# Optimization experiments

Measured on AMD Instinct MI355X. Metric: run time of the kernel, lower is better.

## Reference

```python
import jax, jax.numpy as jnp
import numpy as np

B_, H_, N_, L_ = 4, 512, 64, 2048  # batch, d_model, d_state/2 (conj pairs), seq len


def setup_inputs() -> dict:
    key = jax.random.key(0)
    ks = jax.random.split(key, 8)
    x = jax.random.normal(ks[0], (B_, H_, L_), jnp.float32)
    ln_w = jnp.ones((H_,), jnp.float32)
    ln_b = jnp.zeros((H_,), jnp.float32)
    # S4D-style init: dt log-uniform in [1e-3, 1e-1], A = -1/2 + i*pi*n (S4D-Lin)
    log_dt = jax.random.uniform(ks[1], (H_,), jnp.float32) * (np.log(0.1) - np.log(0.001)) + np.log(0.001)
    log_A_real = jnp.broadcast_to(jnp.log(jnp.float32(0.5)), (H_, N_))
    A_imag = jnp.broadcast_to(np.pi * jnp.arange(N_, dtype=np.float32), (H_, N_))
    B_re = jnp.ones((H_, N_), jnp.float32)
    B_im = jnp.zeros((H_, N_), jnp.float32)
    # 2 kernel channels for bidirectional
    C_re = jax.random.normal(ks[2], (2, H_, N_), jnp.float32) * (0.5 ** 0.5)
    C_im = jax.random.normal(ks[3], (2, H_, N_), jnp.float32) * (0.5 ** 0.5)
    D = jax.random.normal(ks[4], (H_,), jnp.float32)
    W_out = jax.random.normal(ks[5], (H_, H_), jnp.float32) / np.sqrt(H_)
    b_out = jnp.zeros((H_,), jnp.float32)
    return dict(x=x, ln_w=ln_w, ln_b=ln_b, log_dt=log_dt, log_A_real=log_A_real,
                A_imag=A_imag, B_re=B_re, B_im=B_im, C_re=C_re, C_im=C_im,
                D=D, W_out=W_out, b_out=b_out)


def _s4_layer(x, ln_w, ln_b, log_dt, log_A_real, A_imag, B_re, B_im, C_re, C_im, D, W_out, b_out):
    Bb, H, L = x.shape
    # ---- pre-norm LayerNorm over channel dim (module transposes to (B,L,H)) ----
    zt = x.transpose(0, 2, 1)                          # (B, L, H)
    mu = zt.mean(-1, keepdims=True)
    var = jnp.mean((zt - mu) ** 2, -1, keepdims=True)
    zt = (zt - mu) * jax.lax.rsqrt(var + 1e-5) * ln_w + ln_b
    z = zt.transpose(0, 2, 1)                          # (B, H, L)
    # ---- S4 diagonal SSM kernel, ZOH discretization, 2 channels (bidirectional) ----
    dt = jnp.exp(log_dt)[:, None]                      # (H, 1)
    A = -jnp.exp(log_A_real) + 1j * A_imag             # (H, N)
    dtA = A * dt                                       # (H, N)
    dB = (B_re + 1j * B_im) * (jnp.exp(dtA) - 1.0) / A # (H, N) discretized B
    CB = (C_re + 1j * C_im) * dB                       # (2, H, N)
    V = jnp.exp(dtA[:, :, None] * jnp.arange(L))       # (H, N, L) Vandermonde exp(l*dt*A)
    k = 2.0 * jnp.real(jnp.einsum('chn,hnl->chl', CB, V))  # (2, H, L)
    # ---- bidirectional: causal + flipped anticausal kernel, length 2L ----
    zpad = jnp.zeros_like(k[0])
    kb = jnp.concatenate([k[0], zpad], -1) + jnp.concatenate([zpad, k[1][:, ::-1]], -1)  # (H, 2L)
    # ---- FFT convolution ----
    k_f = jnp.fft.rfft(kb, n=2 * L)                    # (H, L+1)
    u_f = jnp.fft.rfft(z, n=2 * L)                     # (B, H, L+1)
    y = jnp.fft.irfft(u_f * k_f, n=2 * L)[..., :L]     # (B, H, L)
    y = y + z * D[:, None]                             # skip connection D*u
    y = jax.nn.gelu(y)                                 # default S4 activation
    y = jnp.einsum('oh,bhl->bol', W_out, y) + b_out[:, None]  # output linear (Conv1d k=1)
    return y + x                                       # residual of S4Layer


def reference(x, ln_w, ln_b, log_dt, log_A_real, A_imag, B_re, B_im, C_re, C_im, D, W_out, b_out):
    return _s4_layer(x, ln_w, ln_b, log_dt, log_A_real, A_imag, B_re, B_im, C_re, C_im, D, W_out, b_out)
```

## Files before the change

kernel.cpp:

```cpp
#include <hip/hip_runtime.h>
#include <math.h>

#define Bq 4
#define Hq 512
#define Nq 64
#define Lq 2048
#define PARAM (Hq*Nq)
#define T 64
#define NC (Lq/T)
#define NCOL 256

__global__ void prep_kernel(const float* __restrict__ log_dt,
                            const float* __restrict__ log_A_real,
                            const float* __restrict__ A_imag,
                            const float* __restrict__ B_re, const float* __restrict__ B_im,
                            const float* __restrict__ C_re, const float* __restrict__ C_im,
                            float* __restrict__ a0, float* __restrict__ b0,
                            float* __restrict__ a1, float* __restrict__ b1,
                            float* __restrict__ pw, float* __restrict__ pwT) {
    int idx = blockIdx.x * blockDim.x + threadIdx.x;
    if (idx >= PARAM) return;
    int h = idx >> 6, n = idx & 63;
    float dt = expf(log_dt[h]);
    float Ar = -expf(log_A_real[idx]);
    float Ai = A_imag[idx];
    float er = expf(Ar * dt);
    float wr = er * cosf(Ai * dt);
    float wi = er * sinf(Ai * dt);
    float mr = wr - 1.0f, mi = wi;
    float den = Ar * Ar + Ai * Ai;
    float qr = (mr * Ar + mi * Ai) / den;
    float qi = (mi * Ar - mr * Ai) / den;
    float Br = B_re[idx], Bi = B_im[idx];
    float dBr = Br * qr - Bi * qi;
    float dBi = Br * qi + Bi * qr;
    float cr = C_re[idx], ci = C_im[idx];
    a0[idx] =  2.0f * (cr * dBr - ci * dBi);
    b0[idx] = -2.0f * (cr * dBi + ci * dBr);
    cr = C_re[PARAM + idx]; ci = C_im[PARAM + idx];
    a1[idx] =  2.0f * (cr * dBr - ci * dBi);
    b1[idx] = -2.0f * (cr * dBi + ci * dBr);
    float c = 1.f, s = 0.f;
    float* base  = pw  + (size_t)h * 65 * 128 + 2 * n;
    float* baseT = pwT + (size_t)(h * 64 + n) * 132;
    for (int d = 0; d <= 64; ++d) {
        *(float2*)(base + (size_t)d * 128) = float2{c, s};
        *(float2*)(baseT + 2 * d)          = float2{c, s};
        float nc = c * wr - s * wi;
        float ns = c * wi + s * wr;
        c = nc; s = ns;
    }
}

__global__ __launch_bounds__(128)
void ktap_kernel(const float* __restrict__ pw,
                 const float* __restrict__ a0, const float* __restrict__ b0,
                 const float* __restrict__ a1, const float* __restrict__ b1,
                 float* __restrict__ kt) {
    int h = blockIdx.x;
    int t = threadIdx.x;
    int dir = t >> 6, d = t & 63;
    const float* aa = dir ? a1 : a0;
    const float* bb = dir ? b1 : b0;
    const float* row = pw + (size_t)(h * 65 + d) * 128;
    float acc = 0.f;
    for (int n = 0; n < 64; ++n) {
        float2 v = *(const float2*)(row + 2 * n);
        acc = fmaf(aa[h * 64 + n], v.x, acc);
        acc = fmaf(bb[h * 64 + n], v.y, acc);
    }
    kt[((size_t)h * 2 + dir) * 64 + d] = acc;
}

__global__ __launch_bounds__(256)
void ln_kernel(const float* __restrict__ x, const float* __restrict__ lnw,
               const float* __restrict__ lnb, float* __restrict__ z) {
    int blk = blockIdx.x;
    int b  = blk / (Lq / 16);
    int l0 = (blk % (Lq / 16)) * 16;
    int tx = threadIdx.x & 15;
    int ty = threadIdx.x >> 4;
    const float* xb = x + (size_t)b * Hq * Lq;
    float s = 0.f, s2 = 0.f;
    for (int h = ty; h < Hq; h += 16) {
        float v = xb[h * Lq + l0 + tx];
        s += v; s2 += v * v;
    }
    __shared__ float rs_[16][17], r2_[16][17], mu_s[16], sg_s[16];
    rs_[ty][tx] = s; r2_[ty][tx] = s2;
    __syncthreads();
    if (ty == 0) {
        float a = 0.f, c = 0.f;
        #pragma unroll
        for (int i = 0; i < 16; ++i) { a += rs_[i][tx]; c += r2_[i][tx]; }
        float mu = a * (1.0f / Hq);
        float var = c * (1.0f / Hq) - mu * mu;
        mu_s[tx] = mu;
        sg_s[tx] = rsqrtf(var + 1e-5f);
    }
    __syncthreads();
    float mu = mu_s[tx], rs = sg_s[tx];
    float* zb = z + (size_t)b * Hq * Lq;
    for (int h = ty; h < Hq; h += 16) {
        float v = xb[h * Lq + l0 + tx];
        zb[h * Lq + l0 + tx] = (v - mu) * rs * lnw[h] + lnb[h];
    }
}

__global__ __launch_bounds__(256, 6)
void delta_kernel(const float* __restrict__ z, const float* __restrict__ pw,
                  float* __restrict__ buf) {
    __shared__ float Bs[64][68];
    int h = blockIdx.x, ct = blockIdx.y;
    int t = threadIdx.x;
    int dir = ct >> 1;
    int cc = t & 31, rb = (t >> 5) & 1, jg = t >> 6;
    int b = (ct & 1) * 2 + rb;
    const float* zb = z + ((size_t)b * Hq + h) * Lq;
    if (dir == 0) {
        #pragma unroll
        for (int f = 0; f < 4; ++f) {
            float4 v = *(const float4*)(zb + cc * 64 + 16 * jg + 4 * f);
            Bs[16*jg+4*f+0][rb*32+cc] = v.x;
            Bs[16*jg+4*f+1][rb*32+cc] = v.y;
            Bs[16*jg+4*f+2][rb*32+cc] = v.z;
            Bs[16*jg+4*f+3][rb*32+cc] = v.w;
        }
    } else {
        #pragma unroll
        for (int f = 0; f < 4; ++f) {
            float4 v = *(const float4*)(zb + 2044 - cc * 64 - 16 * jg - 4 * f);
            Bs[16*jg+4*f+3][rb*32+cc] = v.x;
            Bs[16*jg+4*f+2][rb*32+cc] = v.y;
            Bs[16*jg+4*f+1][rb*32+cc] = v.z;
            Bs[16*jg+4*f+0][rb*32+cc] = v.w;
        }
    }
    __syncthreads();
    int tx = t & 15, ty = t >> 4;
    float aR[4][4] = {}, aI[4][4] = {};
    const float* pwh = pw + (size_t)h * 65 * 128;
    #pragma unroll 4
    for (int kk = 0; kk < 64; ++kk) {
        int d = 63 - kk;
        const float4* pr = (const float4*)(pwh + (size_t)d * 128 + 8 * tx);
        float4 p0 = pr[0], p1 = pr[1];
        float4 bv = *(const float4*)&Bs[kk][4 * ty];
        float pc[4] = {p0.x, p0.z, p1.x, p1.z};
        float ps[4] = {p0.y, p0.w, p1.y, p1.w};
        #pragma unroll
        for (int rr = 0; rr < 4; ++rr) {
            #pragma unroll
            for (int q = 0; q < 4; ++q) {
                aR[rr][q] = fmaf(pc[rr], (&bv.x)[q], aR[rr][q]);
                aI[rr][q] = fmaf(ps[rr], (&bv.x)[q], aI[rr][q]);
            }
        }
    }
    #pragma unroll
    for (int q = 0; q < 4; ++q) {
        int colg = ct * 64 + 4 * ty + q;
        float* dst = buf + ((size_t)h * NCOL + colg) * 128 + 8 * tx;
        float4 v1, v2;
        v1.x = aR[0][q]; v1.y = aI[0][q]; v1.z = aR[1][q]; v1.w = aI[1][q];
        v2.x = aR[2][q]; v2.y = aI[2][q]; v2.z = aR[3][q]; v2.w = aI[3][q];
        *(float4*)dst = v1; *(float4*)(dst + 4) = v2;
    }
}

__global__ __launch_bounds__(256)
void cscan_kernel(const float* __restrict__ pw, float* __restrict__ buf) {
    int e = blockIdx.x * 4 + (threadIdx.x >> 6);
    int n = threadIdx.x & 63;
    int h = e >> 3, dir = (e >> 2) & 1, b = e & 3;
    float2 t64 = *(const float2*)(pw + (size_t)(h * 65 + 64) * 128 + 2 * n);
    float tc = t64.x, ts = t64.y;
    float sr = 0.f, si = 0.f;
    float2* p = (float2*)(buf + ((size_t)h * NCOL + dir * 128 + b * 32) * 128) + n;
    float2 d = p[0];
    for (int c = 0; c < NC; ++c) {
        float2 dn;
        if (c + 1 < NC) dn = p[(c + 1) * 64];
        float2 s; s.x = sr; s.y = si;
        p[c * 64] = s;
        float nr = fmaf(tc, sr, fmaf(-ts, si, d.x));
        float ni = fmaf(ts, sr, fmaf(tc, si, d.y));
        sr = nr; si = ni; d = dn;
    }
}

__global__ __launch_bounds__(256, 4)
void yact_kernel(const float* __restrict__ z, const float* __restrict__ pwT,
                 const float* __restrict__ a0, const float* __restrict__ b0,
                 const float* __restrict__ a1, const float* __restrict__ b1,
                 const float* __restrict__ kt, const float* __restrict__ buf,
                 const float* __restrict__ Dv, float* __restrict__ u) {
    __shared__ float As[64][68];
    __shared__ float Bs[64][68];
    __shared__ float ks0[64], ks1[64], as0_[64], bs0_[64], as1_[64], bs1_[64];
    int h = blockIdx.x, bp = blockIdx.y;
    int t = threadIdx.x;
    if (t < 64) {
        ks0[t]  = kt[((size_t)h * 2 + 0) * 64 + t];
        ks1[t]  = kt[((size_t)h * 2 + 1) * 64 + t];
        as0_[t] = a0[h * 64 + t]; bs0_[t] = b0[h * 64 + t];
        as1_[t] = a1[h * 64 + t]; bs1_[t] = b1[h * 64 + t];
    }
    int tx = t & 15, ty = t >> 4;
    int si = t & 63, kg = t >> 6;
    int bS = 2 * bp + (si >> 5), ch = si & 31;
    const float* zb   = z + ((size_t)bS * Hq + h) * Lq + ch * 64;
    const float* bufh = buf + (size_t)h * NCOL * 128;
    const float* buf0 = bufh + (size_t)(bS * 32 + ch) * 128;
    const float* buf1 = bufh + (size_t)(128 + bS * 32 + (31 - ch)) * 128;
    const float* pwh  = pwT + (size_t)h * 64 * 132;
    float4 rB[4];
    float2 pv[8];
    #pragma unroll
    for (int f = 0; f < 4; ++f)
        rB[f] = *(const float4*)(zb + 16 * kg + 4 * f);
    float acc[4][4] = {};
    __syncthreads();
    for (int p = 0; p < 5; ++p) {
        if (p == 0) {
            #pragma unroll
            for (int q = 0; q < 16; ++q) {
                int kk = 16 * kg + q;
                int d = si - kk;
                As[kk][si] = (d >= 0) ? ks0[d] : ks1[-d - 1];
            }
        } else {
            const float* as_ = (p < 3) ? as0_ : as1_;
            const float* bs_ = (p < 3) ? bs0_ : bs1_;
            #pragma unroll
            for (int q = 0; q < 16; ++q) {
                int j = q >> 1;
                int n = 32 * ((p < 3) ? (p - 1) : (p - 3)) + 8 * kg + j;
                float vx = pv[j].x, vy = pv[j].y;
                As[16 * kg + q][si] = ((q & 1) == 0)
                    ? fmaf(as_[n], vx, bs_[n] * vy)
                    : fmaf(bs_[n], vx, -as_[n] * vy);
            }
        }
        #pragma unroll
        for (int f = 0; f < 4; ++f) {
            Bs[16*kg + 4*f + 0][si] = rB[f].x;
            Bs[16*kg + 4*f + 1][si] = rB[f].y;
            Bs[16*kg + 4*f + 2][si] = rB[f].z;
            Bs[16*kg + 4*f + 3][si] = rB[f].w;
        }
        __syncthreads();
        if (p < 4) {
            int pn = p + 1;
            int pp = (pn < 3) ? (pn - 1) : (pn - 3);
            const float* src = (pn < 3) ? buf0 : buf1;
            #pragma unroll
            for (int f = 0; f < 4; ++f)
                rB[f] = *(const float4*)(src + 64 * pp + 16 * kg + 4 * f);
            int dsel = (pn < 3) ? (si + 1) : (63 - si);
            #pragma unroll
            for (int j = 0; j < 8; ++j) {
                int n = 32 * pp + 8 * kg + j;
                pv[j] = *(const float2*)(pwh + (size_t)n * 132 + 2 * dsel);
            }
        }
        #pragma unroll 8
        for (int kk = 0; kk < 64; ++kk) {
            float4 av = *(const float4*)&As[kk][4 * tx];
            float4 bv = *(const float4*)&Bs[kk][4 * ty];
            #pragma unroll
            for (int ii = 0; ii < 4; ++ii) {
                float a = (&av.x)[ii];
                acc[ii][0] = fmaf(a, bv.x, acc[ii][0]);
                acc[ii][1] = fmaf(a, bv.y, acc[ii][1]);
                acc[ii][2] = fmaf(a, bv.z, acc[ii][2]);
                acc[ii][3] = fmaf(a, bv.w, acc[ii][3]);
            }
        }
        __syncthreads();
    }
    float dv = Dv[h];
    #pragma unroll
    for (int q = 0; q < 4; ++q) {
        int cc2 = 4 * ty + q;
        int b2 = 2 * bp + (cc2 >> 5), ch2 = cc2 & 31;
        size_t base = ((size_t)b2 * Hq + h) * Lq + ch2 * 64 + 4 * tx;
        float4 zr = *(const float4*)(z + base);
        float vv[4];
        vv[0] = acc[0][q] + dv * zr.x;
        vv[1] = acc[1][q] + dv * zr.y;
        vv[2] = acc[2][q] + dv * zr.z;
        vv[3] = acc[3][q] + dv * zr.w;
        #pragma unroll
        for (int i = 0; i < 4; ++i) {
            float v = vv[i];
            float tt = tanhf(0.7978845608028654f * (v + 0.044715f * v * v * v));
            vv[i] = 0.5f * v * (1.0f + tt);
        }
        float4 r; r.x = vv[0]; r.y = vv[1]; r.z = vv[2]; r.w = vv[3];
        *(float4*)(u + base) = r;
    }
}

__global__ __launch_bounds__(256, 1)
void gemm_kernel(const float* __restrict__ u, const float* __restrict__ W,
                 const float* __restrict__ bias, const float* __restrict__ x,
                 float* __restrict__ out) {
    __shared__ float Ws[2][32][132];
    __shared__ float Us[2][32][132];
    int l0 = blockIdx.x * 128;
    int o0 = blockIdx.y * 128;
    int b  = blockIdx.z;
    int t  = threadIdx.x;
    int tx = t & 15, ty = t >> 4;
    const float* ub = u + (size_t)b * Hq * Lq;
    int sf = t & 31, sk = t >> 5;
    int kq = t & 7,  ol = t >> 3;
    float4 su[4], sw[4];
    #pragma unroll
    for (int r = 0; r < 4; ++r)
        su[r] = *(const float4*)(ub + (size_t)(sk + 8*r) * Lq + l0 + 4*sf);
    #pragma unroll
    for (int r = 0; r < 4; ++r)
        sw[r] = *(const float4*)(W + (size_t)(o0 + ol + 32*r) * Hq + 4*kq);
    #pragma unroll
    for (int r = 0; r < 4; ++r)
        *(float4*)&Us[0][sk + 8*r][4*sf] = su[r];
    #pragma unroll
    for (int r = 0; r < 4; ++r) {
        Ws[0][4*kq+0][ol + 32*r] = sw[r].x;
        Ws[0][4*kq+1][ol + 32*r] = sw[r].y;
        Ws[0][4*kq+2][ol + 32*r] = sw[r].z;
        Ws[0][4*kq+3][ol + 32*r] = sw[r].w;
    }
    __syncthreads();
    float acc[2][4][2][4] = {};
    for (int kt = 0; kt < Hq / 32; ++kt) {
        int cur = kt & 1;
        if (kt < 15) {
            int k0 = (kt + 1) * 32;
            #pragma unroll
            for (int r = 0; r < 4; ++r)
                su[r] = *(const float4*)(ub + (size_t)(k0 + sk + 8*r) * Lq + l0 + 4*sf);
            #pragma unroll
            for (int r = 0; r < 4; ++r)
                sw[r] = *(const float4*)(W + (size_t)(o0 + ol + 32*r) * Hq + k0 + 4*kq);
        }
        #pragma unroll 4
        for (int k = 0; k < 32; ++k) {
            float4 a0v = *(const float4*)&Ws[cur][k][4 * tx];
            float4 a1v = *(const float4*)&Ws[cur][k][64 + 4 * tx];
            float4 b0v = *(const float4*)&Us[cur][k][4 * ty];
            float4 b1v = *(const float4*)&Us[cur][k][64 + 4 * ty];
            #pragma unroll
            for (int i = 0; i < 4; ++i) {
                float a0s = (&a0v.x)[i], a1s = (&a1v.x)[i];
                #pragma unroll
                for (int j = 0; j < 4; ++j) {
                    float b0s = (&b0v.x)[j], b1s = (&b1v.x)[j];
                    acc[0][i][0][j] = fmaf(a0s, b0s, acc[0][i][0][j]);
                    acc[0][i][1][j] = fmaf(a0s, b1s, acc[0][i][1][j]);
                    acc[1][i][0][j] = fmaf(a1s, b0s, acc[1][i][0][j]);
                    acc[1][i][1][j] = fmaf(a1s, b1s, acc[1][i][1][j]);
                }
            }
        }
        if (kt < 15) {
            int nxt = cur ^ 1;
            #pragma unroll
            for (int r = 0; r < 4; ++r)
                *(float4*)&Us[nxt][sk + 8*r][4*sf] = su[r];
            #pragma unroll
            for (int r = 0; r < 4; ++r) {
                Ws[nxt][4*kq+0][ol + 32*r] = sw[r].x;
                Ws[nxt][4*kq+1][ol + 32*r] = sw[r].y;
                Ws[nxt][4*kq+2][ol + 32*r] = sw[r].z;
                Ws[nxt][4*kq+3][ol + 32*r] = sw[r].w;
            }
        }
        __syncthreads();
    }
    #pragma unroll
    for (int oq = 0; oq < 2; ++oq) {
        #pragma unroll
        for (int i = 0; i < 4; ++i) {
            int o = o0 + 64 * oq + 4 * tx + i;
            float bo = bias[o];
            #pragma unroll
            for (int lq = 0; lq < 2; ++lq) {
                size_t base = ((size_t)b * Hq + o) * Lq + l0 + 64 * lq + 4 * ty;
                float4 xr = *(const float4*)(x + base);
                float4 r;
                r.x = acc[oq][i][lq][0] + bo + xr.x;
                r.y = acc[oq][i][lq][1] + bo + xr.y;
                r.z = acc[oq][i][lq][2] + bo + xr.z;
                r.w = acc[oq][i][lq][3] + bo + xr.w;
                *(float4*)(out + base) = r;
            }
        }
    }
}

extern "C" void kernel_launch(void* const* d_in, const int* in_sizes, int n_in,
                              void* d_out, int out_size, void* d_ws, size_t ws_size,
                              hipStream_t stream) {
    (void)in_sizes; (void)n_in; (void)out_size; (void)ws_size;
    const float* x          = (const float*)d_in[0];
    const float* ln_w       = (const float*)d_in[1];
    const float* ln_b       = (const float*)d_in[2];
    const float* log_dt     = (const float*)d_in[3];
    const float* log_A_real = (const float*)d_in[4];
    const float* A_imag     = (const float*)d_in[5];
    const float* B_re       = (const float*)d_in[6];
    const float* B_im       = (const float*)d_in[7];
    const float* C_re       = (const float*)d_in[8];
    const float* C_im       = (const float*)d_in[9];
    const float* Dv         = (const float*)d_in[10];
    const float* W          = (const float*)d_in[11];
    const float* b_out      = (const float*)d_in[12];
    float* out = (float*)d_out;
    float* ws  = (float*)d_ws;

    const size_t BHL = (size_t)Bq * Hq * Lq;
    float* a0  = ws;
    float* b0  = ws + (size_t)PARAM;
    float* a1  = ws + 2 * (size_t)PARAM;
    float* b1  = ws + 3 * (size_t)PARAM;
    float* kt  = ws + 4 * (size_t)PARAM;
    float* pw  = ws + 6 * (size_t)PARAM;
    float* pwT = ws + 136 * (size_t)PARAM;
    float* z   = ws + 268 * (size_t)PARAM;
    float* u   = z  + BHL;
    float* buf = u + BHL;

    prep_kernel<<<PARAM / 256, 256, 0, stream>>>(log_dt, log_A_real, A_imag,
                                                 B_re, B_im, C_re, C_im,
                                                 a0, b0, a1, b1, pw, pwT);
    ln_kernel<<<Bq * (Lq / 16), 256, 0, stream>>>(x, ln_w, ln_b, z);
    ktap_kernel<<<Hq, 128, 0, stream>>>(pw, a0, b0, a1, b1, kt);
    delta_kernel<<<dim3(Hq, 4), 256, 0, stream>>>(z, pw, buf);
    cscan_kernel<<<Bq * Hq * 2 / 4, 256, 0, stream>>>(pw, buf);
    yact_kernel<<<dim3(Hq, 2), 256, 0, stream>>>(z, pwT, a0, b0, a1, b1,
                                                 kt, buf, Dv, u);
    gemm_kernel<<<dim3(Lq / 128, Hq / 128, Bq), 256, 0, stream>>>(u, W, b_out, x, out);
}
```

Before: 329.5 us.

## Pre-transpose W and shrink GEMM tile to 128x64 for more blocks

Adds a small kernel that transposes W into the workspace so the GEMM can load W tiles with contiguous float4 stores into shared memory instead of scalar transposed stores. The GEMM tile along L is halved from 128 to 64, which doubles the grid to 512 blocks, cuts the accumulators from 32 to 16 per thread, and the launch bounds now allow 2 blocks per SIMD. The aim is better occupancy and cheaper shared-memory fills. In exchange, each block does less arithmetic per shared-memory load and there is one extra kernel launch.

```diff
diff --git a/kernel.cpp b/kernel.cpp
--- a/kernel.cpp
+++ b/kernel.cpp
@@ -73,6 +73,33 @@
 }
 
 __global__ __launch_bounds__(256)
+void wtrans_kernel(const float* __restrict__ W, float* __restrict__ WT) {
+    __shared__ float tile[64][65];
+    int bo = blockIdx.x * 64;
+    int bk = blockIdx.y * 64;
+    int lx = threadIdx.x & 15;
+    int ly = threadIdx.x >> 4;
+    #pragma unroll
+    for (int r = 0; r < 4; ++r) {
+        float4 v = *(const float4*)(W + (size_t)(bo + ly + 16*r) * Hq + bk + 4*lx);
+        tile[ly + 16*r][4*lx+0] = v.x;
+        tile[ly + 16*r][4*lx+1] = v.y;
+        tile[ly + 16*r][4*lx+2] = v.z;
+        tile[ly + 16*r][4*lx+3] = v.w;
+    }
+    __syncthreads();
+    #pragma unroll
+    for (int r = 0; r < 4; ++r) {
+        float4 v;
+        v.x = tile[4*lx+0][ly + 16*r];
+        v.y = tile[4*lx+1][ly + 16*r];
+        v.z = tile[4*lx+2][ly + 16*r];
+        v.w = tile[4*lx+3][ly + 16*r];
+        *(float4*)(WT + (size_t)(bk + ly + 16*r) * Hq + bo + 4*lx) = v;
+    }
+}
+
+__global__ __launch_bounds__(256)
 void ln_kernel(const float* __restrict__ x, const float* __restrict__ lnw,
                const float* __restrict__ lnb, float* __restrict__ z) {
     int blk = blockIdx.x;
@@ -302,81 +329,70 @@
     }
 }
 
-__global__ __launch_bounds__(256, 1)
-void gemm_kernel(const float* __restrict__ u, const float* __restrict__ W,
+__global__ __launch_bounds__(256, 2)
+void gemm_kernel(const float* __restrict__ u, const float* __restrict__ WT,
                  const float* __restrict__ bias, const float* __restrict__ x,
                  float* __restrict__ out) {
     __shared__ float Ws[2][32][132];
-    __shared__ float Us[2][32][132];
-    int l0 = blockIdx.x * 128;
+    __shared__ float Us[2][32][68];
+    int l0 = blockIdx.x * 64;
     int o0 = blockIdx.y * 128;
     int b  = blockIdx.z;
     int t  = threadIdx.x;
     int tx = t & 15, ty = t >> 4;
     const float* ub = u + (size_t)b * Hq * Lq;
-    int sf = t & 31, sk = t >> 5;
-    int kq = t & 7,  ol = t >> 3;
-    float4 su[4], sw[4];
+    int usf = t & 15, usk = t >> 4;
+    int wsf = t & 31, wsk = t >> 5;
+    float4 su[2], sw[4];
+    #pragma unroll
+    for (int r = 0; r < 2; ++r)
+        su[r] = *(const float4*)(ub + (size_t)(usk + 16*r) * Lq + l0 + 4*usf);
     #pragma unroll
     for (int r = 0; r < 4; ++r)
-        su[r] = *(const float4*)(ub + (size_t)(sk + 8*r) * Lq + l0 + 4*sf);
+        sw[r] = *(const float4*)(WT + (size_t)(wsk + 8*r) * Hq + o0 + 4*wsf);
+    #pragma unroll
+    for (int r = 0; r < 2; ++r)
+        *(float4*)&Us[0][usk + 16*r][4*usf] = su[r];
     #pragma unroll
     for (int r = 0; r < 4; ++r)
-        sw[r] = *(const float4*)(W + (size_t)(o0 + ol + 32*r) * Hq + 4*kq);
-    #pragma unroll
-    for (int r = 0; r < 4; ++r)
-        *(float4*)&Us[0][sk + 8*r][4*sf] = su[r];
-    #pragma unroll
-    for (int r = 0; r < 4; ++r) {
-        Ws[0][4*kq+0][ol + 32*r] = sw[r].x;
-        Ws[0][4*kq+1][ol + 32*r] = sw[r].y;
-        Ws[0][4*kq+2][ol + 32*r] = sw[r].z;
-        Ws[0][4*kq+3][ol + 32*r] = sw[r].w;
-    }
-    __syncthreads();
-    float acc[2][4][2][4] = {};
+        *(float4*)&Ws[0][wsk + 8*r][4*wsf] = sw[r];
+    __syncthreads();
+    float acc[2][4][4] = {};
     for (int kt = 0; kt < Hq / 32; ++kt) {
         int cur = kt & 1;
         if (kt < 15) {
             int k0 = (kt + 1) * 32;
             #pragma unroll
+            for (int r = 0; r < 2; ++r)
+                su[r] = *(const float4*)(ub + (size_t)(k0 + usk + 16*r) * Lq + l0 + 4*usf);
+            #pragma unroll
             for (int r = 0; r < 4; ++r)
-                su[r] = *(const float4*)(ub + (size_t)(k0 + sk + 8*r) * Lq + l0 + 4*sf);
-            #pragma unroll
-            for (int r = 0; r < 4; ++r)
-                sw[r] = *(const float4*)(W + (size_t)(o0 + ol + 32*r) * Hq + k0 + 4*kq);
+                sw[r] = *(const float4*)(WT + (size_t)(k0 + wsk + 8*r) * Hq + o0 + 4*wsf);
         }
         #pragma unroll 4
         for (int k = 0; k < 32; ++k) {
             float4 a0v = *(const float4*)&Ws[cur][k][4 * tx];
             float4 a1v = *(const float4*)&Ws[cur][k][64 + 4 * tx];
-            float4 b0v = *(const float4*)&Us[cur][k][4 * ty];
-            float4 b1v = *(const float4*)&Us[cur][k][64 + 4 * ty];
+            float4 bv  = *(const float4*)&Us[cur][k][4 * ty];
             #pragma unroll
             for (int i = 0; i < 4; ++i) {
                 float a0s = (&a0v.x)[i], a1s = (&a1v.x)[i];
                 #pragma unroll
                 for (int j = 0; j < 4; ++j) {
-                    float b0s = (&b0v.x)[j], b1s = (&b1v.x)[j];
-                    acc[0][i][0][j] = fmaf(a0s, b0s, acc[0][i][0][j]);
-                    acc[0][i][1][j] = fmaf(a0s, b1s, acc[0][i][1][j]);
-                    acc[1][i][0][j] = fmaf(a1s, b0s, acc[1][i][0][j]);
-                    acc[1][i][1][j] = fmaf(a1s, b1s, acc[1][i][1][j]);
+                    float bs = (&bv.x)[j];
+                    acc[0][i][j] = fmaf(a0s, bs, acc[0][i][j]);
+                    acc[1][i][j] = fmaf(a1s, bs, acc[1][i][j]);
                 }
             }
         }
         if (kt < 15) {
             int nxt = cur ^ 1;
             #pragma unroll
+            for (int r = 0; r < 2; ++r)
+                *(float4*)&Us[nxt][usk + 16*r][4*usf] = su[r];
+            #pragma unroll
             for (int r = 0; r < 4; ++r)
-                *(float4*)&Us[nxt][sk + 8*r][4*sf] = su[r];
-            #pragma unroll
-            for (int r = 0; r < 4; ++r) {
-                Ws[nxt][4*kq+0][ol + 32*r] = sw[r].x;
-                Ws[nxt][4*kq+1][ol + 32*r] = sw[r].y;
-                Ws[nxt][4*kq+2][ol + 32*r] = sw[r].z;
-                Ws[nxt][4*kq+3][ol + 32*r] = sw[r].w;
-            }
+                *(float4*)&Ws[nxt][wsk + 8*r][4*wsf] = sw[r];
         }
         __syncthreads();
     }
@@ -386,17 +402,14 @@
         for (int i = 0; i < 4; ++i) {
             int o = o0 + 64 * oq + 4 * tx + i;
             float bo = bias[o];
-            #pragma unroll
-            for (int lq = 0; lq < 2; ++lq) {
-                size_t base = ((size_t)b * Hq + o) * Lq + l0 + 64 * lq + 4 * ty;
-                float4 xr = *(const float4*)(x + base);
-                float4 r;
-                r.x = acc[oq][i][lq][0] + bo + xr.x;
-                r.y = acc[oq][i][lq][1] + bo + xr.y;
-                r.z = acc[oq][i][lq][2] + bo + xr.z;
-                r.w = acc[oq][i][lq][3] + bo + xr.w;
-                *(float4*)(out + base) = r;
-            }
+            size_t base = ((size_t)b * Hq + o) * Lq + l0 + 4 * ty;
+            float4 xr = *(const float4*)(x + base);
+            float4 r;
+            r.x = acc[oq][i][0] + bo + xr.x;
+            r.y = acc[oq][i][1] + bo + xr.y;
+            r.z = acc[oq][i][2] + bo + xr.z;
+            r.w = acc[oq][i][3] + bo + xr.w;
+            *(float4*)(out + base) = r;
         }
     }
 }
@@ -429,7 +442,8 @@
     float* kt  = ws + 4 * (size_t)PARAM;
     float* pw  = ws + 6 * (size_t)PARAM;
     float* pwT = ws + 136 * (size_t)PARAM;
-    float* z   = ws + 268 * (size_t)PARAM;
+    float* wt  = ws + 268 * (size_t)PARAM;
+    float* z   = ws + 276 * (size_t)PARAM;
     float* u   = z  + BHL;
     float* buf = u + BHL;
 
@@ -438,9 +452,10 @@
                                                  a0, b0, a1, b1, pw, pwT);
     ln_kernel<<<Bq * (Lq / 16), 256, 0, stream>>>(x, ln_w, ln_b, z);
     ktap_kernel<<<Hq, 128, 0, stream>>>(pw, a0, b0, a1, b1, kt);
+    wtrans_kernel<<<dim3(Hq / 64, Hq / 64), 256, 0, stream>>>(W, wt);
     delta_kernel<<<dim3(Hq, 4), 256, 0, stream>>>(z, pw, buf);
     cscan_kernel<<<Bq * Hq * 2 / 4, 256, 0, stream>>>(pw, buf);
     yact_kernel<<<dim3(Hq, 2), 256, 0, stream>>>(z, pwT, a0, b0, a1, b1,
                                                  kt, buf, Dv, u);
-    gemm_kernel<<<dim3(Lq / 128, Hq / 128, Bq), 256, 0, stream>>>(u, W, b_out, x, out);
-}
+    gemm_kernel<<<dim3(Lq / 64, Hq / 128, Bq), 256, 0, stream>>>(u, wt, b_out, x, out);
+}
```

New measurement: 332.5 us. About the same (+0.9%).
